# Performance work log

Hardware: AMD Instinct MI355X
Metric: run time of the kernel (lower is better)

The kernel has to match this reference:

```python
import jax, jax.numpy as jnp
import numpy as np

DIM = 2048
HEADS = 16
DIM_HEAD = 128
FF_INNER = DIM * 4
SCALE_BASE = 512
EPS = 1e-5


def setup_inputs() -> dict:
    key = jax.random.key(0)
    k1, k2, k3, k4 = jax.random.split(key, 4)
    fused_out = HEADS * DIM_HEAD + DIM_HEAD + DIM_HEAD + 2 * FF_INNER  # 18688
    x = jax.random.normal(k1, (2, 2048, DIM), dtype=jnp.float32)
    gamma = jnp.ones((DIM,), dtype=jnp.float32)
    W_fused = jax.random.normal(k2, (DIM, fused_out), dtype=jnp.float32) * 0.02
    W_attn_out = jax.random.normal(k3, (HEADS * DIM_HEAD, DIM), dtype=jnp.float32) * 0.02
    W_ff_out = jax.random.normal(k4, (FF_INNER, DIM), dtype=jnp.float32) * 0.02
    return {"x": x, "gamma": gamma, "W_fused": W_fused, "W_attn_out": W_attn_out, "W_ff_out": W_ff_out}


def _rotate_half(t):
    t1, t2 = jnp.split(t, 2, axis=-1)
    return jnp.concatenate((-t2, t1), axis=-1)


def _rotary(n, dtype):
    # RotaryEmbedding with use_xpos=True, scale_base=512
    half = DIM_HEAD // 2
    inv_freq = 1.0 / (10000.0 ** (jnp.arange(0, DIM_HEAD, 2, dtype=dtype) / DIM_HEAD))
    t = jnp.arange(n, dtype=dtype)
    freqs = jnp.einsum('i,j->ij', t, inv_freq)          # [n, half]
    freqs = jnp.concatenate((freqs, freqs), axis=-1)    # [n, dh]
    scale_vec = (jnp.arange(0, DIM_HEAD, 2, dtype=dtype) + 0.4 * DIM_HEAD) / (1.4 * DIM_HEAD)
    power = (t - n // 2) / SCALE_BASE
    scale = scale_vec[None, :] ** power[:, None]        # [n, half]
    scale = jnp.concatenate((scale, scale), axis=-1)    # [n, dh]
    return freqs, scale


def _apply_rope(pos, t, scale):
    return t * jnp.cos(pos) * scale + _rotate_half(t) * jnp.sin(pos) * scale


def reference(x, gamma, W_fused, W_attn_out, W_ff_out):
    b, n, d = x.shape
    # LayerNorm (beta fixed at zero)
    mu = jnp.mean(x, axis=-1, keepdims=True)
    var = jnp.var(x, axis=-1, keepdims=True)
    xn = (x - mu) * jax.lax.rsqrt(var + EPS) * gamma

    proj = xn @ W_fused
    attn_inner = HEADS * DIM_HEAD
    q = proj[..., :attn_inner]
    k = proj[..., attn_inner:attn_inner + DIM_HEAD]
    v = proj[..., attn_inner + DIM_HEAD:attn_inner + 2 * DIM_HEAD]
    ff = proj[..., attn_inner + 2 * DIM_HEAD:]

    q = q.reshape(b, n, HEADS, DIM_HEAD).transpose(0, 2, 1, 3)  # b h n d

    pos, scale = _rotary(n, x.dtype)
    q = _apply_rope(pos, q, scale)            # broadcasts [n,dh] over b,h
    k = _apply_rope(pos, k, 1.0 / scale)      # k is [b, n, dh]

    # multi-query attention, causal
    sim = jnp.einsum('bhid,bjd->bhij', q, k) * (DIM_HEAD ** -0.5)
    causal_mask = jnp.triu(jnp.ones((n, n), dtype=bool), 1)
    sim = jnp.where(causal_mask, jnp.finfo(sim.dtype).min, sim)
    attn = jax.nn.softmax(sim, axis=-1)
    out = jnp.einsum('bhij,bjd->bhid', attn, v)
    out = out.transpose(0, 2, 1, 3).reshape(b, n, attn_inner)
    attn_out = out @ W_attn_out

    # SwiGLU: chunk -> silu(gate) * x
    ff_x, ff_gate = jnp.split(ff, 2, axis=-1)
    ff_out = (jax.nn.silu(ff_gate) * ff_x) @ W_ff_out

    return attn_out + ff_out
```

## Files before the change

kernel.cpp:

```cpp
#include <hip/hip_runtime.h>

typedef __attribute__((ext_vector_type(8))) short short8;
typedef __attribute__((ext_vector_type(4))) float floatx4;
typedef __attribute__((ext_vector_type(8))) unsigned short ushort8;

#define FOUT 18688
#define FFI  8192
#define CATW 10240

__device__ __forceinline__ float b2f(unsigned short u){
  union { unsigned int i; float f; } v; v.i = ((unsigned int)u) << 16; return v.f;
}
__device__ __forceinline__ unsigned short f2b(float f){
  union { float f; unsigned int i; } v; v.f = f;
  unsigned int r = v.i + 0x7FFFu + ((v.i >> 16) & 1u);
  return (unsigned short)(r >> 16);
}
__device__ __forceinline__ void gld_lds16(const void* g, void* l){
  __builtin_amdgcn_global_load_lds((const __attribute__((address_space(1))) void*)g,
                                   (__attribute__((address_space(3))) void*)l, 16, 0, 0);
}

#define SCHED0() __builtin_amdgcn_sched_barrier(0)
#define BARR()   do{ SCHED0(); __builtin_amdgcn_s_barrier(); SCHED0(); }while(0)

__global__ __launch_bounds__(256) void ln_kernel(const float* __restrict__ x,
                                                 const float* __restrict__ gamma,
                                                 unsigned short* __restrict__ xn){
  int row = blockIdx.x;
  const float* xr = x + (size_t)row * 2048;
  int tid = threadIdx.x;
  float v[8]; float s = 0.f, s2 = 0.f;
#pragma unroll
  for(int i=0;i<8;i++){ float t = xr[tid + i*256]; v[i]=t; s+=t; s2+=t*t; }
#pragma unroll
  for(int off=32; off>=1; off>>=1){ s += __shfl_down(s, off, 64); s2 += __shfl_down(s2, off, 64); }
  __shared__ float red[8];
  int wv = tid>>6, ln_ = tid&63;
  if(ln_==0){ red[wv] = s; red[wv+4] = s2; }
  __syncthreads();
  s  = red[0]+red[1]+red[2]+red[3];
  s2 = red[4]+red[5]+red[6]+red[7];
  float mu  = s * (1.f/2048.f);
  float var = s2 * (1.f/2048.f) - mu*mu;
  float rstd = rsqrtf(var + 1e-5f);
#pragma unroll
  for(int i=0;i<8;i++){
    float o = (v[i]-mu)*rstd*gamma[tid + i*256];
    xn[(size_t)row*2048 + tid + i*256] = f2b(o);
  }
}

__global__ __launch_bounds__(256) void tcast64_kernel(const float* __restrict__ W,
                                                      unsigned short* __restrict__ Wt,
                                                      int C, int S, int O){
  __shared__ float t[64][65];
  int bx = blockIdx.x*64;
  int by = blockIdx.y*64;
  int tid = threadIdx.x;
  int r = tid>>2, cq = (tid&3)*16;
  const float* src = W + (size_t)(by + r)*C + bx + cq;
#pragma unroll
  for(int e=0;e<4;e++){
    floatx4 v = *(const floatx4*)(src + e*4);
    t[r][cq+e*4+0]=v[0]; t[r][cq+e*4+1]=v[1]; t[r][cq+e*4+2]=v[2]; t[r][cq+e*4+3]=v[3];
  }
  __syncthreads();
#pragma unroll
  for(int it=0; it<2; it++){
    int s_ = it*256 + tid;
    int c = s_>>3, j8 = s_&7;
    ushort8 o;
#pragma unroll
    for(int e=0;e<8;e++) o[e] = f2b(t[j8*8+e][c]);
    *(ushort8*)&Wt[(size_t)(bx+c)*S + O + by + j8*8] = o;
  }
}

__global__ void vtrans_kernel(const unsigned short* __restrict__ proj, unsigned short* __restrict__ vt){
  __shared__ unsigned short t[32][33];
  int b = blockIdx.z;
  int n0 = blockIdx.x*32, d0 = blockIdx.y*32;
  int tx = threadIdx.x, ty = threadIdx.y;
#pragma unroll
  for(int i=0;i<4;i++) t[ty+i*8][tx] = proj[(size_t)(b*2048 + n0+ty+i*8)*FOUT + 2176 + d0+tx];
  __syncthreads();
#pragma unroll
  for(int i=0;i<4;i++) vt[((size_t)b*128 + d0+ty+i*8)*2048 + n0+tx] = t[tx][ty+i*8];
}

__global__ __launch_bounds__(256) void rope_tab_kernel(floatx4* __restrict__ tab){
  int idx = blockIdx.x*256 + threadIdx.x;
  int i = idx >> 6, j = idx & 63;
  float fj = (float)j, fi = (float)i;
  float p = fi * powf(10000.f, -fj*(1.f/64.f));
  float c = cosf(p), s = sinf(p);
  float sv = (2.f*fj + 51.2f) * (1.f/179.2f);
  float pw = (fi - 1024.f) * (1.f/512.f);
  float sc = powf(sv, pw);
  const float att = 0.08838834764831843f;
  floatx4 o; o[0]=c*sc*att; o[1]=s*sc*att; o[2]=c/sc; o[3]=s/sc;
  tab[idx] = o;
}

__global__ __launch_bounds__(256) void rope_kernel(unsigned short* __restrict__ proj,
                                                   const floatx4* __restrict__ tab){
  int row = blockIdx.x;
  int i = row & 2047;
  int tid = threadIdx.x;
  if(tid >= 136) return;
  int slot = tid >> 3;
  int jc = (tid & 7) * 8;
  unsigned short* pr = proj + (size_t)row*FOUT + ((slot < 16) ? slot*128 : 2048) + jc;
  ushort8 x1 = *(const ushort8*)pr;
  ushort8 x2 = *(const ushort8*)(pr + 64);
  ushort8 o1, o2;
#pragma unroll
  for(int e=0; e<8; e++){
    floatx4 t = tab[i*64 + jc + e];
    float cs = (slot==16) ? t[2] : t[0];
    float ss = (slot==16) ? t[3] : t[1];
    float f1 = b2f(x1[e]);
    float f2 = b2f(x2[e]);
    o1[e] = f2b(f1*cs - f2*ss);
    o2[e] = f2b(f2*cs + f1*ss);
  }
  *(ushort8*)pr = o1;
  *(ushort8*)(pr + 64) = o2;
}

template<int MODE>
__global__ __launch_bounds__(512, 2) void gemm8p_kernel(const unsigned short* __restrict__ A,
                                                        const unsigned short* __restrict__ Bt,
                                                        unsigned short* __restrict__ Cb,
                                                        float* __restrict__ Cf,
                                                        int N, int K, int NT, size_t zstride){
  __shared__ unsigned short lds[65536];
  const int tid = threadIdx.x;
  const int wave = tid>>6, lane = tid&63;
  const int l15 = lane&15, l4 = lane>>4;
  const int wr = wave>>2, wc = wave&3;
  int id = blockIdx.x;
  int cpx = (int)gridDim.x >> 3;
  int swz = (id & 7)*cpx + (id >> 3);
  int tm = swz & 15, tn = swz >> 4;
  int kbase = (int)blockIdx.z * (NT*64);
  const unsigned short* Ab = A  + (size_t)tm*256*K + kbase;
  const unsigned short* Bb = Bt + (size_t)tn*256*K + kbase;
  if(MODE==1) Cf += (size_t)blockIdx.z * zstride;

  const int r0 = tid>>3;
  const int colc = ((tid&7) ^ (r0&7))*8;
  const int dstw = wave*512;

#define STAGE(t_, h_, isB_) do{ \
    const unsigned short* g_ = (isB_) ? Bb : Ab; \
    int db_ = (((t_)&1)<<15) + ((isB_)<<14) + ((h_)<<13) + dstw; \
    gld_lds16(g_ + (size_t)((h_)*128 + r0)*K + (t_)*64 + colc, &lds[db_]); \
    gld_lds16(g_ + (size_t)((h_)*128 + r0 + 64)*K + (t_)*64 + colc, &lds[db_ + 4096]); \
  }while(0)

  const int sw8 = l15&7;
  const int fo0 = ((l4    )^sw8)*8;
  const int fo1 = ((l4 + 4)^sw8)*8;
  const int albase = (wr*128 + l15)*64;
  const int blbase = 16384 + (wc*64 + l15)*64;

#define RD_A4(arr_, buf_, mh_, fo_) do{ \
  _Pragma("unroll") for(int mf=0; mf<4; mf++) \
    arr_[mf] = *(const short8*)&lds[(buf_) + albase + (mh_)*4096 + mf*1024 + (fo_)]; }while(0)
#define RD_B4(arr_, buf_, fo_) do{ \
  _Pragma("unroll") for(int nf=0; nf<4; nf++) \
    arr_[nf] = *(const short8*)&lds[(buf_) + blbase + nf*1024 + (fo_)]; }while(0)
#define MFMA_P(aarr_, barr_, mh_) do{ \
  _Pragma("unroll") for(int mf=0; mf<4; mf++) \
  _Pragma("unroll") for(int nf=0; nf<4; nf++) \
    acc[(mh_)*4+mf][nf] = __builtin_amdgcn_mfma_f32_16x16x32_bf16( \
      aarr_[mf], barr_[nf], acc[(mh_)*4+mf][nf], 0,0,0); }while(0)

  floatx4 acc[8][4];
#pragma unroll
  for(int i=0;i<8;i++)
#pragma unroll
    for(int j=0;j<4;j++) acc[i][j] = (floatx4)0.f;

  STAGE(0,0,0); STAGE(0,1,0); STAGE(0,0,1); STAGE(0,1,1);
  STAGE(1,0,1); STAGE(1,1,1); STAGE(1,0,0);
  asm volatile("s_waitcnt vmcnt(6)" ::: "memory");
  BARR();

  short8 a00_[4], a01_[4], a10_[4], a11_[4], b0_[4], b1_[4];
  for(int t=0; t<NT; ++t){
    const int bufo = (t&1)<<15;
    RD_A4(a00_, bufo, 0, fo0);
    RD_B4(b0_,  bufo, fo0);
    if(t+1 < NT) STAGE(t+1,1,0);
    __builtin_amdgcn_s_setprio(1);
    MFMA_P(a00_, b0_, 0);
    __builtin_amdgcn_s_setprio(0);
    BARR();
    RD_A4(a01_, bufo, 0, fo1);
    RD_B4(b1_,  bufo, fo1);
    if(t+2 < NT) STAGE(t+2,0,1);
    __builtin_amdgcn_s_setprio(1);
    MFMA_P(a01_, b1_, 0);
    __builtin_amdgcn_s_setprio(0);
    BARR();
    RD_A4(a10_, bufo, 1, fo0);
    if(t+2 < NT) STAGE(t+2,1,1);
    __builtin_amdgcn_s_setprio(1);
    MFMA_P(a10_, b0_, 1);
    __builtin_amdgcn_s_setprio(0);
    BARR();
    RD_A4(a11_, bufo, 1, fo1);
    if(t+2 < NT){
      STAGE(t+2,0,0);
      asm volatile("s_waitcnt vmcnt(6)" ::: "memory");
    } else if(t+1 < NT){
      asm volatile("s_waitcnt vmcnt(0)" ::: "memory");
    }
    __builtin_amdgcn_s_setprio(1);
    MFMA_P(a11_, b1_, 1);
    __builtin_amdgcn_s_setprio(0);
    BARR();
  }

#pragma unroll
  for(int m=0;m<8;m++){
#pragma unroll
    for(int n=0;n<4;n++){
#pragma unroll
      for(int r=0;r<4;r++){
        size_t row = (size_t)tm*256 + wr*128 + (m>>2)*64 + (m&3)*16 + l4*4 + r;
        size_t col = (size_t)tn*256 + wc*64 + n*16 + l15;
        float v = acc[m][n][r];
        if(MODE==0)      Cb[row*N + col] = f2b(v);
        else             Cf[row*N + col] = v;
      }
    }
  }
}

__global__ __launch_bounds__(256) void add2_kernel(const float* __restrict__ p0,
                                                   const float* __restrict__ p1,
                                                   float* __restrict__ o, int n4){
  for(int i = blockIdx.x*256 + threadIdx.x; i < n4; i += gridDim.x*256){
    floatx4 a = ((const floatx4*)p0)[i];
    floatx4 b = ((const floatx4*)p1)[i];
    ((floatx4*)o)[i] = a + b;
  }
}

__global__ __launch_bounds__(512) void attn_kernel(const unsigned short* __restrict__ proj,
                                                   const unsigned short* __restrict__ vt,
                                                   unsigned short* __restrict__ ao){
  __shared__ unsigned short lK[2*8192];
  __shared__ unsigned short lV[2*8192];
  __shared__ unsigned short lP[8*1024];
  int qt = (int)gridDim.x - 1 - (int)blockIdx.x;
  int hh = blockIdx.y, b = blockIdx.z;
  int tid = threadIdx.x, wave = tid>>6, lane = tid&63;
  int l15 = lane&15, l4 = lane>>4;
  int q0 = qt*128;
  int qrow = q0 + wave*16 + l15;
  const unsigned short* qp = proj + (size_t)(b*2048 + qrow)*FOUT + hh*128 + l4*8;
  short8 qf[4];
#pragma unroll
  for(int ds=0; ds<4; ds++) qf[ds] = *(const short8*)(qp + ds*32);
  floatx4 po[8];
#pragma unroll
  for(int dt=0; dt<8; dt++) po[dt] = (floatx4)0.f;
  float mrun[4] = {-1e30f,-1e30f,-1e30f,-1e30f};
  float lrun[4] = {0.f,0.f,0.f,0.f};
  unsigned short* lPw = lP + wave*1024;
  const unsigned short* kb = proj + (size_t)(b*2048)*FOUT + 2048;
  const unsigned short* vb = vt + (size_t)b*128*2048;
  int kvmax = 2*qt + 1;

#define STAGE_K(kv_, bo_) do{ \
    _Pragma("unroll") for(int it=0; it<2; it++){ \
      int f = it*512 + tid; \
      int r = f>>4, pc = f&15; \
      int gc = pc ^ (r&7); \
      gld_lds16(kb + (size_t)((kv_)*64 + r)*FOUT + gc*8, &lK[(bo_) + (it*512 + wave*64)*8]); \
    } }while(0)
#define STAGE_V(kv_, bo_) do{ \
    _Pragma("unroll") for(int it=0; it<2; it++){ \
      int f = it*512 + tid; \
      int d = f>>3, pc = f&7; \
      int gc = pc ^ (d&7); \
      gld_lds16(vb + (size_t)d*2048 + (kv_)*64 + gc*8, &lV[(bo_) + (it*512 + wave*64)*8]); \
    } }while(0)

  STAGE_K(0, 0); STAGE_V(0, 0);

  for(int kv=0; kv<=kvmax; kv++){
    int kv0 = kv*64;
    int cb = (kv&1)*8192;
    asm volatile("s_waitcnt vmcnt(0)" ::: "memory");
    __syncthreads();
    if(kv < kvmax){ STAGE_K(kv+1, cb^8192); STAGE_V(kv+1, cb^8192); }
    floatx4 sa[4];
#pragma unroll
    for(int jt=0;jt<4;jt++) sa[jt] = (floatx4)0.f;
#pragma unroll
    for(int jt=0;jt<4;jt++){
      int krow = jt*16 + l15;
#pragma unroll
      for(int ds=0; ds<4; ds++){
        int pc = (l4 + ds*4) ^ (krow&7);
        short8 kf = *(const short8*)&lK[cb + krow*128 + pc*8];
        sa[jt] = __builtin_amdgcn_mfma_f32_16x16x32_bf16(qf[ds], kf, sa[jt], 0,0,0);
      }
    }
    float pv[4][4];
    bool diag = (kv0 + 63 > q0 + wave*16);
#pragma unroll
    for(int jt=0;jt<4;jt++){
#pragma unroll
      for(int r=0;r<4;r++){
        float s = sa[jt][r];
        if(diag && (kv0 + jt*16 + l15 > q0 + wave*16 + l4*4 + r)) s = -1e30f;
        pv[jt][r] = s;
      }
    }
    float mnew[4], corr[4];
#pragma unroll
    for(int r=0;r<4;r++){
      float mx = fmaxf(fmaxf(pv[0][r],pv[1][r]),fmaxf(pv[2][r],pv[3][r]));
      mx = fmaxf(mx, __shfl_xor(mx, 1, 64));
      mx = fmaxf(mx, __shfl_xor(mx, 2, 64));
      mx = fmaxf(mx, __shfl_xor(mx, 4, 64));
      mx = fmaxf(mx, __shfl_xor(mx, 8, 64));
      float mn = fmaxf(mrun[r], mx);
      corr[r] = __expf(mrun[r] - mn);
      mrun[r] = mn;
      mnew[r] = mn;
    }
    float rsum[4] = {0.f,0.f,0.f,0.f};
#pragma unroll
    for(int jt=0;jt<4;jt++){
#pragma unroll
      for(int r=0;r<4;r++){
        float p = __expf(pv[jt][r] - mnew[r]);
        pv[jt][r] = p;
        rsum[r] += p;
      }
    }
#pragma unroll
    for(int r=0;r<4;r++){
      float rs = rsum[r];
      rs += __shfl_xor(rs, 1, 64);
      rs += __shfl_xor(rs, 2, 64);
      rs += __shfl_xor(rs, 4, 64);
      rs += __shfl_xor(rs, 8, 64);
      lrun[r] = lrun[r]*corr[r] + rs;
    }
#pragma unroll
    for(int dt=0;dt<8;dt++){
#pragma unroll
      for(int r=0;r<4;r++) po[dt][r] *= corr[r];
    }
#pragma unroll
    for(int jt=0;jt<4;jt++){
#pragma unroll
      for(int r=0;r<4;r++){
        int i_ = l4*4 + r;
        int j = jt*16 + l15;
        int pc = (j>>3) ^ (i_&7);
        lPw[i_*64 + pc*8 + (j&7)] = f2b(pv[jt][r]);
      }
    }
    asm volatile("s_waitcnt lgkmcnt(0)" ::: "memory");
    short8 pf[2];
#pragma unroll
    for(int ks=0;ks<2;ks++){
      int pc = (l4 + ks*4) ^ (l15&7);
      pf[ks] = *(const short8*)&lPw[l15*64 + pc*8];
    }
#pragma unroll
    for(int dt=0;dt<8;dt++){
      int d = dt*16 + l15;
#pragma unroll
      for(int ks=0;ks<2;ks++){
        int pc = (ks*4 + l4) ^ (d&7);
        short8 vf = *(const short8*)&lV[cb + d*64 + pc*8];
        po[dt] = __builtin_amdgcn_mfma_f32_16x16x32_bf16(pf[ks], vf, po[dt], 0,0,0);
      }
    }
  }
#pragma unroll
  for(int r=0;r<4;r++){
    float inv = 1.f / lrun[r];
    size_t orow = (size_t)(b*2048 + q0 + wave*16 + l4*4 + r);
#pragma unroll
    for(int dt=0;dt<8;dt++){
      ao[orow*CATW + hh*128 + dt*16 + l15] = f2b(po[dt][r]*inv);
    }
  }
}

__global__ __launch_bounds__(256) void swiglu_kernel(const unsigned short* __restrict__ proj,
                                                     unsigned short* __restrict__ cat){
  size_t idx = (size_t)blockIdx.x*256 + threadIdx.x;
  int row = (int)(idx >> 10);
  int c8  = (int)(idx & 1023);
  const unsigned short* pr = proj + (size_t)row*FOUT + 2304 + c8*8;
  ushort8 xv = *(const ushort8*)pr;
  ushort8 gv = *(const ushort8*)(pr + FFI);
  ushort8 ov;
#pragma unroll
  for(int e=0;e<8;e++){
    float xf = b2f(xv[e]);
    float gf = b2f(gv[e]);
    float sg = gf / (1.f + __expf(-gf));
    ov[e] = f2b(sg*xf);
  }
  *(ushort8*)(cat + (size_t)row*CATW + 2048 + c8*8) = ov;
}

extern "C" void kernel_launch(void* const* d_in, const int* in_sizes, int n_in,
                              void* d_out, int out_size, void* d_ws, size_t ws_size,
                              hipStream_t stream){
  const float* x     = (const float*)d_in[0];
  const float* gamma = (const float*)d_in[1];
  const float* Wf    = (const float*)d_in[2];
  const float* Wa    = (const float*)d_in[3];
  const float* Wff   = (const float*)d_in[4];
  float* out = (float*)d_out;

  char* p = (char*)d_ws;
  unsigned short* xn    = (unsigned short*)p;  p += (size_t)4096*2048*2;
  unsigned short* WfT   = (unsigned short*)p;  p += (size_t)18688*2048*2;
  unsigned short* proj  = (unsigned short*)p;  p += (size_t)4096*18688*2;
  unsigned short* BtCat = (unsigned short*)p;  p += (size_t)2048*CATW*2;
  unsigned short* cat   = (unsigned short*)p;  p += (size_t)4096*CATW*2;
  unsigned short* vtb   = (unsigned short*)p;  p += (size_t)2*128*2048*2;
  floatx4*        rtab  = (floatx4*)p;         p += (size_t)2048*64*16;
  float* part = (float*)d_ws;

  ln_kernel<<<4096, 256, 0, stream>>>(x, gamma, xn);
  rope_tab_kernel<<<512, 256, 0, stream>>>(rtab);
  tcast64_kernel<<<dim3(292,32),  256, 0, stream>>>(Wf,  WfT,   18688, 2048, 0);
  tcast64_kernel<<<dim3(32,32),   256, 0, stream>>>(Wa,  BtCat, 2048,  CATW, 0);
  tcast64_kernel<<<dim3(32,128),  256, 0, stream>>>(Wff, BtCat, 2048,  CATW, 2048);
  gemm8p_kernel<0><<<dim3(1168,1,1), 512, 0, stream>>>(xn, WfT, proj, nullptr, 18688, 2048, 32, 0);
  rope_kernel<<<4096, 256, 0, stream>>>(proj, rtab);
  vtrans_kernel<<<dim3(64,4,2), dim3(32,8), 0, stream>>>(proj, vtb);
  attn_kernel<<<dim3(16,16,2), 512, 0, stream>>>(proj, vtb, cat);
  swiglu_kernel<<<16384, 256, 0, stream>>>(proj, cat);
  gemm8p_kernel<1><<<dim3(128,1,2), 512, 0, stream>>>(cat, BtCat, nullptr, part, 2048, 10240, 80,
                                                      (size_t)4096*2048);
  add2_kernel<<<2048, 256, 0, stream>>>(part, part + (size_t)4096*2048, out, 2097152);
}
```

Measured before the change: 739.7 us.

## Replace 256x256 ping-pong GEMM with 256x128 tile, K=32 triple-buffered GEMM

Both GEMMs switch from a 512-thread 256x256 tile with K-step 64, double buffering and four sub-phases per step to a 256-thread 256x128 tile with K-step 32 and a three-stage LDS ring buffer. Each step now does one read phase and one barrier. Operands are swapped in the MFMA so each lane holds four consecutive output columns, which allows vectorized 8-byte bf16 or 16-byte fp32 stores. This cuts LDS use and barrier count and may raise occupancy, but each tile reuses less data and the grid gets larger.

```diff
diff --git a/kernel.cpp b/kernel.cpp
--- a/kernel.cpp
+++ b/kernel.cpp
@@ -3,6 +3,7 @@
 typedef __attribute__((ext_vector_type(8))) short short8;
 typedef __attribute__((ext_vector_type(4))) float floatx4;
 typedef __attribute__((ext_vector_type(8))) unsigned short ushort8;
+typedef __attribute__((ext_vector_type(2))) unsigned int uint2v;
 
 #define FOUT 18688
 #define FFI  8192
@@ -130,53 +131,43 @@
 }
 
 template<int MODE>
-__global__ __launch_bounds__(512, 2) void gemm8p_kernel(const unsigned short* __restrict__ A,
+__global__ __launch_bounds__(256, 2) void gemm2r_kernel(const unsigned short* __restrict__ A,
                                                         const unsigned short* __restrict__ Bt,
                                                         unsigned short* __restrict__ Cb,
                                                         float* __restrict__ Cf,
                                                         int N, int K, int NT, size_t zstride){
-  __shared__ unsigned short lds[65536];
+  __shared__ unsigned short lds[36864];
   const int tid = threadIdx.x;
   const int wave = tid>>6, lane = tid&63;
   const int l15 = lane&15, l4 = lane>>4;
-  const int wr = wave>>2, wc = wave&3;
+  const int wr = wave>>1, wc = wave&1;
   int id = blockIdx.x;
   int cpx = (int)gridDim.x >> 3;
   int swz = (id & 7)*cpx + (id >> 3);
   int tm = swz & 15, tn = swz >> 4;
-  int kbase = (int)blockIdx.z * (NT*64);
+  int kbase = (int)blockIdx.z * (NT*32);
   const unsigned short* Ab = A  + (size_t)tm*256*K + kbase;
-  const unsigned short* Bb = Bt + (size_t)tn*256*K + kbase;
+  const unsigned short* Bb = Bt + (size_t)tn*128*K + kbase;
   if(MODE==1) Cf += (size_t)blockIdx.z * zstride;
 
-  const int r0 = tid>>3;
-  const int colc = ((tid&7) ^ (r0&7))*8;
-  const int dstw = wave*512;
-
-#define STAGE(t_, h_, isB_) do{ \
-    const unsigned short* g_ = (isB_) ? Bb : Ab; \
-    int db_ = (((t_)&1)<<15) + ((isB_)<<14) + ((h_)<<13) + dstw; \
-    gld_lds16(g_ + (size_t)((h_)*128 + r0)*K + (t_)*64 + colc, &lds[db_]); \
-    gld_lds16(g_ + (size_t)((h_)*128 + r0 + 64)*K + (t_)*64 + colc, &lds[db_ + 4096]); \
+#define STG(t_, bufo_) do{ \
+    _Pragma("unroll") for(int i_=0;i_<4;i_++){ \
+      int s_ = i_*256 + tid; \
+      int r_ = s_>>2, cs_ = s_&3; \
+      gld_lds16(Ab + (size_t)r_*K + (t_)*32 + (cs_^((r_>>1)&3))*8, \
+                &lds[(bufo_) + (i_*256 + wave*64)*8]); \
+    } \
+    _Pragma("unroll") for(int i_=0;i_<2;i_++){ \
+      int s_ = i_*256 + tid; \
+      int r_ = s_>>2, cs_ = s_&3; \
+      gld_lds16(Bb + (size_t)r_*K + (t_)*32 + (cs_^((r_>>1)&3))*8, \
+                &lds[(bufo_) + 8192 + (i_*256 + wave*64)*8]); \
+    } \
   }while(0)
 
-  const int sw8 = l15&7;
-  const int fo0 = ((l4    )^sw8)*8;
-  const int fo1 = ((l4 + 4)^sw8)*8;
-  const int albase = (wr*128 + l15)*64;
-  const int blbase = 16384 + (wc*64 + l15)*64;
-
-#define RD_A4(arr_, buf_, mh_, fo_) do{ \
-  _Pragma("unroll") for(int mf=0; mf<4; mf++) \
-    arr_[mf] = *(const short8*)&lds[(buf_) + albase + (mh_)*4096 + mf*1024 + (fo_)]; }while(0)
-#define RD_B4(arr_, buf_, fo_) do{ \
-  _Pragma("unroll") for(int nf=0; nf<4; nf++) \
-    arr_[nf] = *(const short8*)&lds[(buf_) + blbase + nf*1024 + (fo_)]; }while(0)
-#define MFMA_P(aarr_, barr_, mh_) do{ \
-  _Pragma("unroll") for(int mf=0; mf<4; mf++) \
-  _Pragma("unroll") for(int nf=0; nf<4; nf++) \
-    acc[(mh_)*4+mf][nf] = __builtin_amdgcn_mfma_f32_16x16x32_bf16( \
-      aarr_[mf], barr_[nf], acc[(mh_)*4+mf][nf], 0,0,0); }while(0)
+  const int fo = (l4 ^ ((l15>>1)&3))*8;
+  const int albase = (wr*128 + l15)*32;
+  const int blbase = 8192 + (wc*64 + l15)*32;
 
   floatx4 acc[8][4];
 #pragma unroll
@@ -184,58 +175,48 @@
 #pragma unroll
     for(int j=0;j<4;j++) acc[i][j] = (floatx4)0.f;
 
-  STAGE(0,0,0); STAGE(0,1,0); STAGE(0,0,1); STAGE(0,1,1);
-  STAGE(1,0,1); STAGE(1,1,1); STAGE(1,0,0);
+  STG(0, 0); STG(1, 12288);
   asm volatile("s_waitcnt vmcnt(6)" ::: "memory");
   BARR();
 
-  short8 a00_[4], a01_[4], a10_[4], a11_[4], b0_[4], b1_[4];
+  int bufo = 0, sbo = 24576;
   for(int t=0; t<NT; ++t){
-    const int bufo = (t&1)<<15;
-    RD_A4(a00_, bufo, 0, fo0);
-    RD_B4(b0_,  bufo, fo0);
-    if(t+1 < NT) STAGE(t+1,1,0);
+    short8 a_[8], b_[4];
+#pragma unroll
+    for(int mf=0; mf<8; mf++) a_[mf] = *(const short8*)&lds[bufo + albase + mf*512 + fo];
+#pragma unroll
+    for(int nf=0; nf<4; nf++) b_[nf] = *(const short8*)&lds[bufo + blbase + nf*512 + fo];
+    if(t+2 < NT) STG(t+2, sbo);
     __builtin_amdgcn_s_setprio(1);
-    MFMA_P(a00_, b0_, 0);
+#pragma unroll
+    for(int mf=0; mf<8; mf++)
+#pragma unroll
+      for(int nf=0; nf<4; nf++)
+        acc[mf][nf] = __builtin_amdgcn_mfma_f32_16x16x32_bf16(b_[nf], a_[mf], acc[mf][nf], 0,0,0);
     __builtin_amdgcn_s_setprio(0);
+    if(t+2 < NT){      asm volatile("s_waitcnt vmcnt(6)" ::: "memory"); }
+    else if(t+1 < NT){ asm volatile("s_waitcnt vmcnt(0)" ::: "memory"); }
     BARR();
-    RD_A4(a01_, bufo, 0, fo1);
-    RD_B4(b1_,  bufo, fo1);
-    if(t+2 < NT) STAGE(t+2,0,1);
-    __builtin_amdgcn_s_setprio(1);
-    MFMA_P(a01_, b1_, 0);
-    __builtin_amdgcn_s_setprio(0);
-    BARR();
-    RD_A4(a10_, bufo, 1, fo0);
-    if(t+2 < NT) STAGE(t+2,1,1);
-    __builtin_amdgcn_s_setprio(1);
-    MFMA_P(a10_, b0_, 1);
-    __builtin_amdgcn_s_setprio(0);
-    BARR();
-    RD_A4(a11_, bufo, 1, fo1);
-    if(t+2 < NT){
-      STAGE(t+2,0,0);
-      asm volatile("s_waitcnt vmcnt(6)" ::: "memory");
-    } else if(t+1 < NT){
-      asm volatile("s_waitcnt vmcnt(0)" ::: "memory");
-    }
-    __builtin_amdgcn_s_setprio(1);
-    MFMA_P(a11_, b1_, 1);
-    __builtin_amdgcn_s_setprio(0);
-    BARR();
-  }
-
-#pragma unroll
-  for(int m=0;m<8;m++){
-#pragma unroll
-    for(int n=0;n<4;n++){
-#pragma unroll
-      for(int r=0;r<4;r++){
-        size_t row = (size_t)tm*256 + wr*128 + (m>>2)*64 + (m&3)*16 + l4*4 + r;
-        size_t col = (size_t)tn*256 + wc*64 + n*16 + l15;
-        float v = acc[m][n][r];
-        if(MODE==0)      Cb[row*N + col] = f2b(v);
-        else             Cf[row*N + col] = v;
+    bufo += 12288; if(bufo == 36864) bufo = 0;
+    sbo  += 12288; if(sbo  == 36864) sbo  = 0;
+  }
+
+  const size_t crow0 = (size_t)tm*256 + wr*128 + l15;
+  const size_t ccol0 = (size_t)tn*128 + wc*64 + l4*4;
+#pragma unroll
+  for(int mf=0; mf<8; mf++){
+    size_t row = crow0 + mf*16;
+#pragma unroll
+    for(int nf=0; nf<4; nf++){
+      size_t col = ccol0 + nf*16;
+      floatx4 v = acc[mf][nf];
+      if(MODE==0){
+        uint2v u;
+        u[0] = (unsigned int)f2b(v[0]) | ((unsigned int)f2b(v[1])<<16);
+        u[1] = (unsigned int)f2b(v[2]) | ((unsigned int)f2b(v[3])<<16);
+        *(uint2v*)&Cb[row*N + col] = u;
+      } else {
+        *(floatx4*)&Cf[row*N + col] = v;
       }
     }
   }
@@ -444,12 +425,12 @@
   tcast64_kernel<<<dim3(292,32),  256, 0, stream>>>(Wf,  WfT,   18688, 2048, 0);
   tcast64_kernel<<<dim3(32,32),   256, 0, stream>>>(Wa,  BtCat, 2048,  CATW, 0);
   tcast64_kernel<<<dim3(32,128),  256, 0, stream>>>(Wff, BtCat, 2048,  CATW, 2048);
-  gemm8p_kernel<0><<<dim3(1168,1,1), 512, 0, stream>>>(xn, WfT, proj, nullptr, 18688, 2048, 32, 0);
+  gemm2r_kernel<0><<<dim3(2336,1,1), 256, 0, stream>>>(xn, WfT, proj, nullptr, 18688, 2048, 64, 0);
   rope_kernel<<<4096, 256, 0, stream>>>(proj, rtab);
   vtrans_kernel<<<dim3(64,4,2), dim3(32,8), 0, stream>>>(proj, vtb);
   attn_kernel<<<dim3(16,16,2), 512, 0, stream>>>(proj, vtb, cat);
   swiglu_kernel<<<16384, 256, 0, stream>>>(proj, cat);
-  gemm8p_kernel<1><<<dim3(128,1,2), 512, 0, stream>>>(cat, BtCat, nullptr, part, 2048, 10240, 80,
+  gemm2r_kernel<1><<<dim3(256,1,2), 256, 0, stream>>>(cat, BtCat, nullptr, part, 2048, 10240, 160,
                                                       (size_t)4096*2048);
   add2_kernel<<<2048, 256, 0, stream>>>(part, part + (size_t)4096*2048, out, 2097152);
 }
```

After: 840.1 us. 13.6% more time.
